# Kernel optimization log

Measured on AMD Instinct MI355X. Metric: run time of the kernel, lower is better.

The kernel has to match this reference:

```python
import jax, jax.numpy as jnp
import numpy as np

GROUPS = 4
EPS = 1e-5

def _bn(x, p, axis=1):
    # p: (4, C) rows = gamma, beta, running_mean, running_var (inference BN)
    g, b, m, v = p
    shp = [1] * x.ndim
    shp[axis] = -1
    return (x - m.reshape(shp)) * (g.reshape(shp) / jnp.sqrt(v.reshape(shp) + EPS)) + b.reshape(shp)

def _axial(x, qkv_w, bn_qkv, bn_sim, bn_out, rel, width):
    # x: (N, C, H, W). Attend along H if width=False, along W if width=True.
    if width:
        x = x.transpose(0, 2, 1, 3)   # (N, H, C, W)
    else:
        x = x.transpose(0, 3, 1, 2)   # (N, W, C, H)
    N, Wd, C, H = x.shape
    gp = C // GROUPS
    x = x.reshape(N * Wd, C, H)
    qkv = jnp.einsum('oc,bch->boh', qkv_w, x)            # 1x1 conv1d
    qkv = _bn(qkv, bn_qkv, axis=1)
    qkv = qkv.reshape(N * Wd, GROUPS, 2 * gp, H)
    q, k, v = qkv[:, :, :gp // 2], qkv[:, :, gp // 2:gp], qkv[:, :, gp:]
    i = jnp.arange(H)
    rel_idx = i[:, None] - i[None, :] + H - 1             # (H, H)
    all_emb = rel[:, rel_idx]                             # (2*gp, H, H)
    q_emb, k_emb, v_emb = all_emb[:gp // 2], all_emb[gp // 2:gp], all_emb[gp:]
    qr = jnp.einsum('bgci,cij->bgij', q, q_emb) * 0.1     # f_qr = 0.1
    kr = jnp.einsum('bgci,cij->bgij', k, k_emb).swapaxes(2, 3) * 0.1  # f_kr
    qk = jnp.einsum('bgci,bgcj->bgij', q, k)
    stacked = jnp.concatenate([qk, qr, kr], axis=1)       # (NW, 3*groups, H, H)
    stacked = _bn(stacked, bn_sim, axis=1)
    sim = stacked.reshape(N * Wd, 3, GROUPS, H, H).sum(1)
    sim = jax.nn.softmax(sim, axis=3)
    sv = jnp.einsum('bgij,bgcj->bgci', sim, v)            # f_sv = 1.0
    sve = jnp.einsum('bgij,cij->bgci', sim, v_emb) * 0.1  # f_sve = 0.1
    out = jnp.concatenate([sv, sve], axis=-1).reshape(N * Wd, 2 * C, H)
    out = _bn(out, bn_out, axis=1)
    out = out.reshape(N, Wd, C, 2, H).sum(3)              # (N, Wd, C, H)
    if width:
        return out.transpose(0, 2, 1, 3)                  # (N, C, H, W)
    return out.transpose(0, 2, 3, 1)

def _conv3x3(x, w, b):
    y = jax.lax.conv_general_dilated(x, w, (1, 1), 'SAME',
                                     dimension_numbers=('NCHW', 'OIHW', 'NCHW'))
    return y + b[None, :, None, None]

def setup_inputs() -> dict:
    key = jax.random.key(0)
    ks = jax.random.split(key, 16)
    C, KS = 256, 44
    def bn_pack(k, c):
        p = jax.random.uniform(k, (4, c), dtype=jnp.float32)
        return p.at[3].add(0.5)  # keep running_var well away from 0
    return {
        'x': jax.random.normal(ks[0], (16, C, 2 * KS, 2 * KS), jnp.float32),
        'h_qkv_w': jax.random.normal(ks[1], (2 * C, C), jnp.float32) * np.sqrt(1.0 / C),
        'h_bn_qkv': bn_pack(ks[2], 2 * C),
        'h_bn_sim': bn_pack(ks[3], 3 * GROUPS),
        'h_bn_out': bn_pack(ks[4], 2 * C),
        'h_rel': jax.random.normal(ks[5], (2 * (C // GROUPS), 2 * KS - 1), jnp.float32) * np.sqrt(GROUPS / C),
        'w_qkv_w': jax.random.normal(ks[6], (2 * C, C), jnp.float32) * np.sqrt(1.0 / C),
        'w_bn_qkv': bn_pack(ks[7], 2 * C),
        'w_bn_sim': bn_pack(ks[8], 3 * GROUPS),
        'w_bn_out': bn_pack(ks[9], 2 * C),
        'w_rel': jax.random.normal(ks[10], (2 * (C // GROUPS), 2 * KS - 1), jnp.float32) * np.sqrt(GROUPS / C),
        'conv_w': jax.random.normal(ks[11], (C, C, 3, 3), jnp.float32) * np.sqrt(1.0 / (C * 9)),
        'conv_b': jax.random.normal(ks[12], (C,), jnp.float32) * 0.01,
    }

def reference(x, h_qkv_w, h_bn_qkv, h_bn_sim, h_bn_out, h_rel,
              w_qkv_w, w_bn_qkv, w_bn_sim, w_bn_out, w_rel, conv_w, conv_b):
    B, C, H2, W2 = x.shape
    h, w = H2 // 2, W2 // 2
    # 'b c (p1 h)(p2 w) -> (b p1 p2) c h w'; same axial blocks applied to all 4 patches
    p = x.reshape(B, C, 2, h, 2, w).transpose(0, 2, 4, 1, 3, 5).reshape(B * 4, C, h, w)
    r = p
    p = _axial(p, h_qkv_w, h_bn_qkv, h_bn_sim, h_bn_out, h_rel, width=False)
    p = _axial(p, w_qkv_w, w_bn_qkv, w_bn_sim, w_bn_out, w_rel, width=True)
    p = p + r
    p = _conv3x3(p, conv_w, conv_b)
    # '(b p1 p2) c h w -> b c (p1 h)(p2 w)'
    out = p.reshape(B, 2, 2, C, h, w).transpose(0, 3, 1, 4, 2, 5).reshape(B, C, H2, W2)
    return out
```

## Files before the change

### kernel.cpp

```cpp
#include <hip/hip_runtime.h>
#include <math.h>

#define EPSV 1e-5f

typedef unsigned short u16t;
typedef unsigned int u32t;
typedef __attribute__((ext_vector_type(8))) short bf16x8;
typedef __attribute__((ext_vector_type(8))) unsigned short u16x8;
typedef __attribute__((ext_vector_type(4))) float f32x4;

#define N_P  31719424
#define N_CW 589824
#define N_QW 131072

__device__ __align__(16) u16t g_cwhi[N_CW], g_cwlo[N_CW];
__device__ __align__(16) u16t g_qwhi[2][N_QW], g_qwlo[2][N_QW];
__device__ __align__(16) u16t g_relq[2][3072];
__device__ __align__(16) u16t g_relk[2][3072];
__device__ __align__(16) u16t g_relv[2][6144];

__device__ __forceinline__ u16t f2bf_rn(float f) {
    u32t u = __float_as_uint(f);
    u32t r = u + 0x7FFFu + ((u >> 16) & 1u);
    return (u16t)(r >> 16);
}
__device__ __forceinline__ float bf2f(u16t h) {
    return __uint_as_float(((u32t)h) << 16);
}

__global__ __launch_bounds__(256)
void transpose_x(const float* __restrict__ x,
                 u16t* __restrict__ xth, u16t* __restrict__ xtl)
{
    __shared__ u16t th[64][90];
    __shared__ u16t tl[64][90];
    const int cg = blockIdx.x, yy = blockIdx.y, b = blockIdx.z;
    const int t = threadIdx.x;
    const float* src = x + ((size_t)(b * 256 + cg * 64) * 88 + yy) * 88;
    for (int e = t; e < 5632; e += 256) {
        int c = e / 88, xx = e - c * 88;
        float v = src[(size_t)c * 7744 + xx];
        u16t hi = f2bf_rn(v);
        u16t lo = f2bf_rn(v - bf2f(hi));
        th[c][xx] = hi;
        tl[c][xx] = lo;
    }
    __syncthreads();
    const int i2 = (yy >= 44);
    const int yl = yy - 44 * i2;
    for (int u = t; u < 5632; u += 256) {
        int xx = u >> 6, c = u & 63;
        int i4 = (xx >= 44);
        int xl = xx - 44 * i4;
        int n = b * 4 + i2 * 2 + i4;
        size_t idx = ((size_t)(n * 44 + yl) * 44 + xl) * 256 + cg * 64 + c;
        xth[idx] = th[c][xx];
        xtl[idx] = tl[c][xx];
    }
}

__global__ __launch_bounds__(256)
void wsplit_conv(const float* __restrict__ cw)
{
    int idx = blockIdx.x * 256 + threadIdx.x;
    if (idx >= N_CW) return;
    int tap = idx % 9;
    int rem = idx / 9;
    int ci = rem & 255, co = rem >> 8;
    float w = cw[idx];
    u16t hi = f2bf_rn(w);
    u16t lo = f2bf_rn(w - bf2f(hi));
    int cit = ci >> 5, ci5 = ci & 31, ci8 = ci5 >> 3, e = ci5 & 7;
    int didx = (((cit * 9 + tap) * 4 + ci8) * 256 + co) * 8 + e;
    g_cwhi[didx] = hi;
    g_cwlo[didx] = lo;
}

__global__ __launch_bounds__(256)
void wsplit_qkv(const float* __restrict__ wh_, const float* __restrict__ ww_)
{
    int idx = blockIdx.x * 256 + threadIdx.x;
    if (idx >= 2 * N_QW) return;
    int sel = idx >> 17;
    int id  = idx & (N_QW - 1);
    float w = (sel ? ww_ : wh_)[id];
    u16t hi = f2bf_rn(w);
    u16t lo = f2bf_rn(w - bf2f(hi));
    int o = id >> 8, c = id & 255;
    int kt = c >> 5, ci8 = (c >> 3) & 3, e = c & 7;
    int didx = ((kt * 4 + ci8) * 512 + o) * 8 + e;
    g_qwhi[sel][didx] = hi;
    g_qwlo[sel][didx] = lo;
}

__global__ __launch_bounds__(256)
void wsplit_rel(const float* __restrict__ rh, const float* __restrict__ rw)
{
    int idx = blockIdx.x * 256 + threadIdx.x;
    if (idx >= 24576) return;
    int sel = idx >= 12288;
    int id  = idx - sel * 12288;
    const float* rel = sel ? rw : rh;
    if (id < 3072) {
        int d = id >> 5, c = id & 31;
        g_relq[sel][id] = (d < 87) ? f2bf_rn(rel[c * 87 + d]) : (u16t)0;
    } else if (id < 6144) {
        int j = id - 3072;
        int d = j >> 5, c = j & 31;
        g_relk[sel][j] = (d < 87) ? f2bf_rn(rel[(32 + c) * 87 + d]) : (u16t)0;
    } else {
        int j = id - 6144;
        int c = j / 96, d = j - c * 96;
        g_relv[sel][j] = (d < 87) ? f2bf_rn(rel[(64 + c) * 87 + d]) : (u16t)0;
    }
}

#define OFF_XL 24576
#define OFF_QH 0
#define OFF_QL 3072
#define OFF_KH 6144
#define OFF_KL 9216
#define OFF_VH 12288
#define OFF_VL 20480
#define OFF_PH 28672
#define OFF_PL 34816
#define OFF_KR 28672
#define OFF_RB 40960
#define OFF_SC 50176

template<int WIDTH>
__global__ __launch_bounds__(256, 2)
void axial_kernel(const u16t* __restrict__ sh, const u16t* __restrict__ sl,
                  const u16t* __restrict__ resh, const u16t* __restrict__ resl,
                  u16t* __restrict__ outh, u16t* __restrict__ outl,
                  int sel,
                  const float* __restrict__ bnq,
                  const float* __restrict__ bns,
                  const float* __restrict__ bno)
{
    __shared__ __align__(128) char smem[62720];

    const int blk = blockIdx.x;
    const int n   = blk / 44;
    const int col = blk - n * 44;
    const int t = threadIdx.x;
    const int wv = t >> 6, lane = t & 63;
    const int l15 = lane & 15, l16 = lane >> 4;

    if (!WIDTH) {
        for (int e = t; e < 6144; e += 256) {
            int i = e >> 7, cp = e & 127;
            u32t vH = 0, vL = 0;
            if (i < 44) {
                size_t s0 = ((size_t)(n * 44 + i) * 44 + col) * 256 + cp * 2;
                vH = *(const u32t*)(sh + s0);
                vL = *(const u32t*)(sl + s0);
            }
            u32t a = ((u32t)(i * 512 + cp * 4)) ^ (((u32t)(i & 7)) << 4);
            *(u32t*)(smem + a) = vH;
            *(u32t*)(smem + OFF_XL + a) = vL;
        }
    } else {
        const u16t* ph = sh + (size_t)(n * 44 + col) * 44 * 256;
        const u16t* pl = sl + (size_t)(n * 44 + col) * 44 * 256;
        for (int e = t; e < 6144; e += 256) {
            int i = e >> 7, cp = e & 127;
            u32t vH = 0, vL = 0;
            if (i < 44) {
                vH = *(const u32t*)(ph + i * 256 + cp * 2);
                vL = *(const u32t*)(pl + i * 256 + cp * 2);
            }
            u32t a = ((u32t)(i * 512 + cp * 4)) ^ (((u32t)(i & 7)) << 4);
            *(u32t*)(smem + a) = vH;
            *(u32t*)(smem + OFF_XL + a) = vL;
        }
    }
    __syncthreads();

    f32x4 acc[8][3];
    #pragma unroll
    for (int mf = 0; mf < 8; ++mf)
        #pragma unroll
        for (int nf = 0; nf < 3; ++nf) acc[mf][nf] = (f32x4)0.f;
    {
        const u16t* WH = g_qwhi[sel];
        const u16t* WL = g_qwlo[sel];
        for (int kt = 0; kt < 8; ++kt) {
            bf16x8 bh[3], bl[3];
            #pragma unroll
            for (int nf = 0; nf < 3; ++nf) {
                int i = nf * 16 + l15;
                u32t a = ((u32t)(i * 512 + kt * 64 + l16 * 16)) ^ (((u32t)(i & 7)) << 4);
                bh[nf] = *(const bf16x8*)(smem + a);
                bl[nf] = *(const bf16x8*)(smem + OFF_XL + a);
            }
            #pragma unroll
            for (int mf = 0; mf < 8; ++mf) {
                int o = (mf * 4 + wv) * 16 + l15;
                size_t wb = ((size_t)(kt * 4 + l16) * 512 + o) * 8;
                bf16x8 ah = *(const bf16x8*)(WH + wb);
                bf16x8 al = *(const bf16x8*)(WL + wb);
                #pragma unroll
                for (int nf = 0; nf < 3; ++nf) {
                    acc[mf][nf] = __builtin_amdgcn_mfma_f32_16x16x32_bf16(ah, bh[nf], acc[mf][nf], 0, 0, 0);
                    acc[mf][nf] = __builtin_amdgcn_mfma_f32_16x16x32_bf16(al, bh[nf], acc[mf][nf], 0, 0, 0);
                    acc[mf][nf] = __builtin_amdgcn_mfma_f32_16x16x32_bf16(ah, bl[nf], acc[mf][nf], 0, 0, 0);
                }
            }
        }
    }
    __syncthreads();

    for (int e = t; e < 1280; e += 256) {
        int arr = e & 1, q = e >> 1;
        int c = q / 10, k = q - c * 10;
        u32t ad = ((u32t)(c * 128 + 88 + k * 4)) ^ (((u32t)(c & 7)) << 4);
        *(u32t*)(smem + (arr ? OFF_VL : OFF_VH) + ad) = 0;
    }

    for (int g = 0; g < 4; ++g) {
        f32x4 fq[3], fv[3];
        #pragma unroll
        for (int nf = 0; nf < 3; ++nf) { fq[nf] = acc[0][nf]; fv[nf] = acc[1][nf]; }
        #pragma unroll
        for (int m = 1; m < 4; ++m) {
            if (g == m) {
                #pragma unroll
                for (int nf = 0; nf < 3; ++nf) { fq[nf] = acc[2 * m][nf]; fv[nf] = acc[2 * m + 1][nf]; }
            }
        }

        #pragma unroll
        for (int r = 0; r < 4; ++r) {
            int ol = wv * 16 + l16 * 4 + r;
            {
                int o = g * 128 + ol;
                float s = bnq[o] * rsqrtf(bnq[1536 + o] + EPSV);
                float h = bnq[512 + o] - bnq[1024 + o] * s;
                #pragma unroll
                for (int nf = 0; nf < 3; ++nf) {
                    int i = nf * 16 + l15;
                    float val = fq[nf][r] * s + h;
                    u16t hi = f2bf_rn(val);
                    u16t lo = f2bf_rn(val - bf2f(hi));
                    if (ol < 32) {
                        u32t a = ((u32t)(i * 64 + ol * 2)) ^ (((u32t)(i & 7)) << 4);
                        *(u16t*)(smem + OFF_QH + a) = hi;
                        *(u16t*)(smem + OFF_QL + a) = lo;
                    } else {
                        int c = ol - 32;
                        u32t a = ((u32t)(i * 64 + c * 2)) ^ (((u32t)(i & 7)) << 4);
                        *(u16t*)(smem + OFF_KH + a) = hi;
                        *(u16t*)(smem + OFF_KL + a) = lo;
                    }
                }
            }
            {
                int c = ol;
                int o = g * 128 + 64 + c;
                float s = bnq[o] * rsqrtf(bnq[1536 + o] + EPSV);
                float h = bnq[512 + o] - bnq[1024 + o] * s;
                #pragma unroll
                for (int nf = 0; nf < 3; ++nf) {
                    int i = nf * 16 + l15;
                    if (i < 44) {
                        float val = fv[nf][r] * s + h;
                        u16t hi = f2bf_rn(val);
                        u16t lo = f2bf_rn(val - bf2f(hi));
                        u32t a = ((u32t)(c * 128 + i * 2)) ^ (((u32t)(c & 7)) << 4);
                        *(u16t*)(smem + OFF_VH + a) = hi;
                        *(u16t*)(smem + OFF_VL + a) = lo;
                    }
                }
            }
        }
        __syncthreads();

        for (int f = wv; f < 9; f += 4) {
            int mf = f / 3, nf = f % 3;
            int ia = mf * 16 + l15;
            u32t aq = ((u32t)(ia * 64 + l16 * 16)) ^ (((u32t)(ia & 7)) << 4);
            bf16x8 qh = *(const bf16x8*)(smem + OFF_QH + aq);
            bf16x8 ql = *(const bf16x8*)(smem + OFF_QL + aq);
            int jb = nf * 16 + l15;
            u32t ak = ((u32t)(jb * 64 + l16 * 16)) ^ (((u32t)(jb & 7)) << 4);
            bf16x8 kh = *(const bf16x8*)(smem + OFF_KH + ak);
            bf16x8 kl = *(const bf16x8*)(smem + OFF_KL + ak);
            f32x4 d = (f32x4)0.f;
            d = __builtin_amdgcn_mfma_f32_16x16x32_bf16(qh, kh, d, 0, 0, 0);
            d = __builtin_amdgcn_mfma_f32_16x16x32_bf16(ql, kh, d, 0, 0, 0);
            d = __builtin_amdgcn_mfma_f32_16x16x32_bf16(qh, kl, d, 0, 0, 0);
            #pragma unroll
            for (int r = 0; r < 4; ++r) {
                int i = mf * 16 + l16 * 4 + r;
                *(float*)(smem + OFF_SC + (i * 49 + nf * 16 + l15) * 4) = d[r];
            }
        }
        for (int f = wv; f < 18; f += 4) {
            int mf = f / 6, nf = f % 6;
            int ia = mf * 16 + l15;
            u32t aq = ((u32t)(ia * 64 + l16 * 16)) ^ (((u32t)(ia & 7)) << 4);
            bf16x8 qh = *(const bf16x8*)(smem + OFF_QH + aq);
            bf16x8 rb = *(const bf16x8*)(&g_relq[sel][(nf * 16 + l15) * 32 + l16 * 8]);
            f32x4 d = (f32x4)0.f;
            d = __builtin_amdgcn_mfma_f32_16x16x32_bf16(qh, rb, d, 0, 0, 0);
            #pragma unroll
            for (int r = 0; r < 4; ++r) {
                int i = mf * 16 + l16 * 4 + r;
                u32t a = ((u32t)(i * 192 + (nf * 16 + l15) * 2)) ^ (((u32t)(i & 7)) << 4);
                *(u16t*)(smem + OFF_RB + a) = f2bf_rn(d[r]);
            }
        }
        for (int f = wv; f < 18; f += 4) {
            int mf = f / 6, nf = f % 6;
            int ja = mf * 16 + l15;
            u32t ak = ((u32t)(ja * 64 + l16 * 16)) ^ (((u32t)(ja & 7)) << 4);
            bf16x8 kh = *(const bf16x8*)(smem + OFF_KH + ak);
            bf16x8 rb = *(const bf16x8*)(&g_relk[sel][(nf * 16 + l15) * 32 + l16 * 8]);
            f32x4 d = (f32x4)0.f;
            d = __builtin_amdgcn_mfma_f32_16x16x32_bf16(kh, rb, d, 0, 0, 0);
            #pragma unroll
            for (int r = 0; r < 4; ++r) {
                int j = mf * 16 + l16 * 4 + r;
                u32t a = ((u32t)(j * 192 + (nf * 16 + l15) * 2)) ^ (((u32t)(j & 7)) << 4);
                *(u16t*)(smem + OFF_KR + a) = f2bf_rn(d[r]);
            }
        }
        __syncthreads();

        {
            const float sqk = bns[g]     * rsqrtf(bns[36 + g] + EPSV);
            const float sqr = bns[4 + g] * rsqrtf(bns[40 + g] + EPSV);
            const float skr = bns[8 + g] * rsqrtf(bns[44 + g] + EPSV);
            for (int e = t; e < 1936; e += 256) {
                int i = e / 44, j = e - i * 44;
                int dq = i - j + 43, dk = j - i + 43;
                float scv = *(const float*)(smem + OFF_SC + (i * 49 + j) * 4);
                u16t rq = *(const u16t*)(smem + OFF_RB + (((u32t)(i * 192 + dq * 2)) ^ (((u32t)(i & 7)) << 4)));
                u16t rk = *(const u16t*)(smem + OFF_KR + (((u32t)(j * 192 + dk * 2)) ^ (((u32t)(j & 7)) << 4)));
                *(float*)(smem + OFF_SC + (i * 49 + j) * 4) =
                    sqk * scv + 0.1f * (sqr * bf2f(rq) + skr * bf2f(rk));
            }
        }
        __syncthreads();

        for (int i = wv; i < 44; i += 4) {
            float v = (lane < 44) ? *(const float*)(smem + OFF_SC + (i * 49 + lane) * 4) : -INFINITY;
            float m = v;
            #pragma unroll
            for (int off = 32; off; off >>= 1) m = fmaxf(m, __shfl_xor(m, off));
            float ex = (lane < 44) ? __expf(v - m) : 0.f;
            float ssum = ex;
            #pragma unroll
            for (int off = 32; off; off >>= 1) ssum += __shfl_xor(ssum, off);
            if (lane < 44) *(float*)(smem + OFF_SC + (i * 49 + lane) * 4) = ex / ssum;
        }
        __syncthreads();

        for (int e = t; e < 3072; e += 256) {
            int i = e >> 6, j = e & 63;
            float v = (i < 44 && j < 44) ? *(const float*)(smem + OFF_SC + (i * 49 + j) * 4) : 0.f;
            u16t hi = f2bf_rn(v);
            u16t lo = f2bf_rn(v - bf2f(hi));
            u32t a = ((u32t)(i * 128 + j * 2)) ^ (((u32t)(i & 7)) << 4);
            *(u16t*)(smem + OFF_PH + a) = hi;
            *(u16t*)(smem + OFF_PL + a) = lo;
        }
        for (int e = t; e < 4608; e += 256) {
            int i = e / 96, d = e - i * 96;
            int j = i - d + 43;
            u16t v = 0;
            if (i < 44 && j >= 0 && j < 44)
                v = f2bf_rn(*(const float*)(smem + OFF_SC + (i * 49 + j) * 4));
            u32t a = ((u32t)(i * 192 + d * 2)) ^ (((u32t)(i & 7)) << 4);
            *(u16t*)(smem + OFF_RB + a) = v;
        }
        __syncthreads();

        {
            f32x4 svf[3], svef[3];
            int fi = 0;
            for (int f = wv; f < 12; f += 4, ++fi) {
                int mf = f / 3, nf = f % 3;
                f32x4 dsv = (f32x4)0.f, dsve = (f32x4)0.f;
                #pragma unroll
                for (int kt = 0; kt < 2; ++kt) {
                    int ca = mf * 16 + l15;
                    u32t av = ((u32t)(ca * 128 + kt * 64 + l16 * 16)) ^ (((u32t)(ca & 7)) << 4);
                    bf16x8 vh = *(const bf16x8*)(smem + OFF_VH + av);
                    bf16x8 vl = *(const bf16x8*)(smem + OFF_VL + av);
                    int ib = nf * 16 + l15;
                    u32t ap = ((u32t)(ib * 128 + kt * 64 + l16 * 16)) ^ (((u32t)(ib & 7)) << 4);
                    bf16x8 ph = *(const bf16x8*)(smem + OFF_PH + ap);
                    bf16x8 pl = *(const bf16x8*)(smem + OFF_PL + ap);
                    dsv = __builtin_amdgcn_mfma_f32_16x16x32_bf16(vh, ph, dsv, 0, 0, 0);
                    dsv = __builtin_amdgcn_mfma_f32_16x16x32_bf16(vl, ph, dsv, 0, 0, 0);
                    dsv = __builtin_amdgcn_mfma_f32_16x16x32_bf16(vh, pl, dsv, 0, 0, 0);
                }
                #pragma unroll
                for (int kt = 0; kt < 3; ++kt) {
                    int ca = mf * 16 + l15;
                    bf16x8 ar = *(const bf16x8*)(&g_relv[sel][ca * 96 + kt * 32 + l16 * 8]);
                    int ib = nf * 16 + l15;
                    u32t as = ((u32t)(ib * 192 + kt * 64 + l16 * 16)) ^ (((u32t)(ib & 7)) << 4);
                    bf16x8 s2 = *(const bf16x8*)(smem + OFF_RB + as);
                    dsve = __builtin_amdgcn_mfma_f32_16x16x32_bf16(ar, s2, dsve, 0, 0, 0);
                }
                svf[fi] = dsv; svef[fi] = dsve;
            }
            __syncthreads();
            fi = 0;
            for (int f = wv; f < 12; f += 4, ++fi) {
                int mf = f / 3, nf = f % 3;
                #pragma unroll
                for (int r = 0; r < 4; ++r) {
                    int c = mf * 16 + l16 * 4 + r;
                    int o0 = g * 128 + 2 * c;
                    float s0 = bno[o0]     * rsqrtf(bno[1536 + o0] + EPSV);
                    float h0 = bno[512 + o0] - bno[1024 + o0] * s0;
                    float s1 = bno[o0 + 1] * rsqrtf(bno[1537 + o0] + EPSV);
                    float h1 = bno[513 + o0] - bno[1025 + o0] * s1;
                    int i = nf * 16 + l15;
                    float val = s0 * svf[fi][r] + h0 + s1 * (0.1f * svef[fi][r]) + h1;
                    *(float*)(smem + OFF_SC + (c * 49 + i) * 4) = val;
                }
            }
        }
        __syncthreads();

        for (int e = t; e < 2816; e += 256) {
            int c = e & 63, i = e >> 6;
            float val = *(const float*)(smem + OFF_SC + (c * 49 + i) * 4);
            int cf = g * 64 + c;
            size_t idx;
            if (!WIDTH) {
                idx = ((size_t)(n * 44 + i) * 44 + col) * 256 + cf;
            } else {
                idx = ((size_t)(n * 44 + col) * 44 + i) * 256 + cf;
                val += bf2f(resh[idx]) + bf2f(resl[idx]);
            }
            u16t hi = f2bf_rn(val);
            u16t lo = f2bf_rn(val - bf2f(hi));
            outh[idx] = hi;
            outl[idx] = lo;
        }
        __syncthreads();
    }
}

__global__ __launch_bounds__(256)
void conv_kernel(const u16t* __restrict__ phi,
                 const u16t* __restrict__ plo,
                 const float* __restrict__ cb,
                 float* __restrict__ out)
{
    __shared__ __align__(16) u16t Xs2[2][4 * 50 * 32];

    const int yb = blockIdx.x, n = blockIdx.y;
    const int y0 = yb * 2;
    const int b = n >> 2, i2 = (n >> 1) & 1, i4 = n & 1;
    const int t = threadIdx.x;
    const int wv = t >> 6, lane = t & 63;
    const int l15 = lane & 15, l16 = lane >> 4;

    f32x4 acc[4][6];
    #pragma unroll
    for (int mf = 0; mf < 4; ++mf)
        #pragma unroll
        for (int nf = 0; nf < 6; ++nf) acc[mf][nf] = (f32x4)0.f;

    char* lds = (char*)&Xs2[0][0];

    for (int cit = 0; cit < 8; ++cit) {
        const int ci0 = cit * 32;
        __syncthreads();
        for (int m = t; m < 1600; m += 256) {
            int ci8 = m & 3;
            int rem = m >> 2;
            int colm = rem % 50;
            int rr  = rem / 50;
            int arr = rr >> 2, rowidx = rr & 3;
            int gy = y0 - 1 + rowidx, gx = colm - 1;
            u16x8 v = (u16x8)0;
            if (gy >= 0 && gy < 44 && gx >= 0 && gx < 44) {
                const u16t* src = (arr ? plo : phi)
                    + (size_t)((n * 44 + gy) * 44 + gx) * 256 + ci0 + ci8 * 8;
                v = *(const u16x8*)src;
            }
            u32t addr = (u32t)((rowidx * 50 + colm) * 64 + ci8 * 16);
            addr ^= ((colm & 7) << 4);
            *(u16x8*)(lds + arr * 12800 + addr) = v;
        }
        __syncthreads();

        for (int tap = 0; tap < 9; ++tap) {
            const int dy = tap / 3, dx = tap % 3;
            const size_t wb = ((size_t)((cit * 9 + tap) * 4 + l16) * 256 + wv * 64 + l15) * 8;
            const u16x8* wh = (const u16x8*)(g_cwhi + wb);
            const u16x8* wl = (const u16x8*)(g_cwlo + wb);
            bf16x8 ah[4], al[4];
            #pragma unroll
            for (int mf = 0; mf < 4; ++mf) {
                ah[mf] = (bf16x8)wh[mf * 16];
                al[mf] = (bf16x8)wl[mf * 16];
            }
            int colr = l15 + dx;
            u32t rbase = (u32t)((dy * 50 + colr) * 64 + l16 * 16);
            rbase ^= ((colr & 7) << 4);
            const char* hb = lds + rbase;

            #pragma unroll
            for (int nf = 0; nf < 6; ++nf) {
                const int ry = nf / 3, cbk = nf % 3;
                const int off = ry * 3200 + cbk * 1024;
                bf16x8 bh = *(const bf16x8*)(hb + off);
                bf16x8 bl = *(const bf16x8*)(hb + 12800 + off);
                #pragma unroll
                for (int mf = 0; mf < 4; ++mf) {
                    acc[mf][nf] = __builtin_amdgcn_mfma_f32_16x16x32_bf16(ah[mf], bh, acc[mf][nf], 0, 0, 0);
                    acc[mf][nf] = __builtin_amdgcn_mfma_f32_16x16x32_bf16(al[mf], bh, acc[mf][nf], 0, 0, 0);
                    acc[mf][nf] = __builtin_amdgcn_mfma_f32_16x16x32_bf16(ah[mf], bl, acc[mf][nf], 0, 0, 0);
                }
            }
        }
    }

    #pragma unroll
    for (int mf = 0; mf < 4; ++mf) {
        const int cobase = wv * 64 + mf * 16 + l16 * 4;
        float bias[4];
        #pragma unroll
        for (int r = 0; r < 4; ++r) bias[r] = cb[cobase + r];
        #pragma unroll
        for (int nf = 0; nf < 6; ++nf) {
            const int ry = nf / 3, cbk = nf % 3;
            const int x = cbk * 16 + l15;
            if (x < 44) {
                const int y = y0 + ry;
                #pragma unroll
                for (int r = 0; r < 4; ++r) {
                    const int co = cobase + r;
                    out[((size_t)(b * 256 + co) * 88 + i2 * 44 + y) * 88 + i4 * 44 + x]
                        = acc[mf][nf][r] + bias[r];
                }
            }
        }
    }
}

extern "C" void kernel_launch(void* const* d_in, const int* in_sizes, int n_in,
                              void* d_out, int out_size, void* d_ws, size_t ws_size,
                              hipStream_t stream)
{
    (void)in_sizes; (void)n_in; (void)out_size; (void)ws_size;

    const float* x        = (const float*)d_in[0];
    const float* h_qkv_w  = (const float*)d_in[1];
    const float* h_bn_qkv = (const float*)d_in[2];
    const float* h_bn_sim = (const float*)d_in[3];
    const float* h_bn_out = (const float*)d_in[4];
    const float* h_rel    = (const float*)d_in[5];
    const float* w_qkv_w  = (const float*)d_in[6];
    const float* w_bn_qkv = (const float*)d_in[7];
    const float* w_bn_sim = (const float*)d_in[8];
    const float* w_bn_out = (const float*)d_in[9];
    const float* w_rel    = (const float*)d_in[10];
    const float* conv_w   = (const float*)d_in[11];
    const float* conv_b   = (const float*)d_in[12];

    u16t* xth = (u16t*)d_ws;
    u16t* xtl = xth + N_P;
    u16t* p1h = xtl + N_P;
    u16t* p1l = p1h + N_P;
    float* o  = (float*)d_out;

    transpose_x<<<dim3(4, 88, 16), 256, 0, stream>>>(x, xth, xtl);
    wsplit_conv<<<(N_CW + 255) / 256, 256, 0, stream>>>(conv_w);
    wsplit_qkv<<<(2 * N_QW + 255) / 256, 256, 0, stream>>>(h_qkv_w, w_qkv_w);
    wsplit_rel<<<96, 256, 0, stream>>>(h_rel, w_rel);

    axial_kernel<0><<<2816, 256, 0, stream>>>(xth, xtl, nullptr, nullptr, p1h, p1l,
        0, h_bn_qkv, h_bn_sim, h_bn_out);
    axial_kernel<1><<<2816, 256, 0, stream>>>(p1h, p1l, xth, xtl, p1h, p1l,
        1, w_bn_qkv, w_bn_sim, w_bn_out);
    conv_kernel<<<dim3(22, 64), 256, 0, stream>>>(p1h, p1l, conv_b, o);
}
```

Baseline: 1.780 ms.

## Restructure axial attention: precompute BN, scatter rel terms, fuse output epilogue

Folds the batch-norm scale and shift factors, including the 0.1 relative-embedding factors, into a small preprocessing kernel so the axial kernel no longer recomputes rsqrt per element. The qr/kr relative terms stay in registers and are added into the score matrix with LDS atomics, replacing the bf16 staging buffers and the separate combine pass. Softmax now writes the hi/lo probability split and the diagonal-shifted buffer directly. The output BN, residual add and stores are fused into the MFMA epilogue with vectorized writes. Less shared memory lets occupancy go from 2 to 3 blocks. The cost is LDS atomic contention and higher register pressure.

After: 2.172 ms. 1.22x slower.

```diff
diff --git a/kernel.cpp b/kernel.cpp
--- a/kernel.cpp
+++ b/kernel.cpp
@@ -7,6 +7,7 @@
 typedef unsigned int u32t;
 typedef __attribute__((ext_vector_type(8))) short bf16x8;
 typedef __attribute__((ext_vector_type(8))) unsigned short u16x8;
+typedef __attribute__((ext_vector_type(4))) unsigned short u16x4;
 typedef __attribute__((ext_vector_type(4))) float f32x4;
 
 #define N_P  31719424
@@ -18,6 +19,9 @@
 __device__ __align__(16) u16t g_relq[2][3072];
 __device__ __align__(16) u16t g_relk[2][3072];
 __device__ __align__(16) u16t g_relv[2][6144];
+__device__ __align__(16) float g_bnq_s[2][512], g_bnq_h[2][512];
+__device__ __align__(16) float g_out_s0[2][256], g_out_s1[2][256], g_out_h[2][256];
+__device__ float g_bnsf[2][12];
 
 __device__ __forceinline__ u16t f2bf_rn(float f) {
     u32t u = __float_as_uint(f);
@@ -111,7 +115,40 @@
     } else {
         int j = id - 6144;
         int c = j / 96, d = j - c * 96;
-        g_relv[sel][j] = (d < 87) ? f2bf_rn(rel[(64 + c) * 87 + d]) : (u16t)0;
+        g_relv[sel][j] = (d < 87) ? f2bf_rn(0.1f * rel[(64 + c) * 87 + d]) : (u16t)0;
+    }
+}
+
+__global__ __launch_bounds__(256)
+void wsplit_bn(const float* __restrict__ hq, const float* __restrict__ hs, const float* __restrict__ ho,
+               const float* __restrict__ wq, const float* __restrict__ ws, const float* __restrict__ wo)
+{
+    int idx = blockIdx.x * 256 + threadIdx.x;
+    if (idx >= 1560) return;
+    int sel = idx >= 780;
+    int id  = idx - sel * 780;
+    const float* bq = sel ? wq : hq;
+    const float* bs = sel ? ws : hs;
+    const float* bo = sel ? wo : ho;
+    if (id < 512) {
+        float s = bq[id] * rsqrtf(bq[1536 + id] + EPSV);
+        g_bnq_s[sel][id] = s;
+        g_bnq_h[sel][id] = bq[512 + id] - bq[1024 + id] * s;
+    } else if (id < 768) {
+        int cf = id - 512;
+        int o0 = 2 * cf, o1 = o0 + 1;
+        float s0 = bo[o0] * rsqrtf(bo[1536 + o0] + EPSV);
+        float s1 = bo[o1] * rsqrtf(bo[1536 + o1] + EPSV);
+        g_out_s0[sel][cf] = s0;
+        g_out_s1[sel][cf] = s1;
+        g_out_h[sel][cf] = (bo[512 + o0] - bo[1024 + o0] * s0)
+                         + (bo[512 + o1] - bo[1024 + o1] * s1);
+    } else {
+        int k = id - 768;
+        int gg = k & 3, which = k >> 2;
+        float s = bs[which * 4 + gg] * rsqrtf(bs[36 + which * 4 + gg] + EPSV);
+        if (which) s *= 0.1f;
+        g_bnsf[sel][which * 4 + gg] = s;
     }
 }
 
@@ -124,21 +161,17 @@
 #define OFF_VL 20480
 #define OFF_PH 28672
 #define OFF_PL 34816
-#define OFF_KR 28672
-#define OFF_RB 40960
-#define OFF_SC 50176
+#define OFF_SC 40960
+#define OFF_S2 0
 
 template<int WIDTH>
-__global__ __launch_bounds__(256, 2)
+__global__ __launch_bounds__(256, 3)
 void axial_kernel(const u16t* __restrict__ sh, const u16t* __restrict__ sl,
                   const u16t* __restrict__ resh, const u16t* __restrict__ resl,
                   u16t* __restrict__ outh, u16t* __restrict__ outl,
-                  int sel,
-                  const float* __restrict__ bnq,
-                  const float* __restrict__ bns,
-                  const float* __restrict__ bno)
-{
-    __shared__ __align__(128) char smem[62720];
+                  int sel)
+{
+    __shared__ __align__(128) char smem[50384];
 
     const int blk = blockIdx.x;
     const int n   = blk / 44;
@@ -146,6 +179,7 @@
     const int t = threadIdx.x;
     const int wv = t >> 6, lane = t & 63;
     const int l15 = lane & 15, l16 = lane >> 4;
+    float* SCf = (float*)(smem + OFF_SC);
 
     if (!WIDTH) {
         for (int e = t; e < 6144; e += 256) {
@@ -235,8 +269,7 @@
             int ol = wv * 16 + l16 * 4 + r;
             {
                 int o = g * 128 + ol;
-                float s = bnq[o] * rsqrtf(bnq[1536 + o] + EPSV);
-                float h = bnq[512 + o] - bnq[1024 + o] * s;
+                float s = g_bnq_s[sel][o], h = g_bnq_h[sel][o];
                 #pragma unroll
                 for (int nf = 0; nf < 3; ++nf) {
                     int i = nf * 16 + l15;
@@ -258,8 +291,7 @@
             {
                 int c = ol;
                 int o = g * 128 + 64 + c;
-                float s = bnq[o] * rsqrtf(bnq[1536 + o] + EPSV);
-                float h = bnq[512 + o] - bnq[1024 + o] * s;
+                float s = g_bnq_s[sel][o], h = g_bnq_h[sel][o];
                 #pragma unroll
                 for (int nf = 0; nf < 3; ++nf) {
                     int i = nf * 16 + l15;
@@ -276,76 +308,76 @@
         }
         __syncthreads();
 
-        for (int f = wv; f < 9; f += 4) {
-            int mf = f / 3, nf = f % 3;
-            int ia = mf * 16 + l15;
-            u32t aq = ((u32t)(ia * 64 + l16 * 16)) ^ (((u32t)(ia & 7)) << 4);
-            bf16x8 qh = *(const bf16x8*)(smem + OFF_QH + aq);
-            bf16x8 ql = *(const bf16x8*)(smem + OFF_QL + aq);
-            int jb = nf * 16 + l15;
-            u32t ak = ((u32t)(jb * 64 + l16 * 16)) ^ (((u32t)(jb & 7)) << 4);
-            bf16x8 kh = *(const bf16x8*)(smem + OFF_KH + ak);
-            bf16x8 kl = *(const bf16x8*)(smem + OFF_KL + ak);
-            f32x4 d = (f32x4)0.f;
-            d = __builtin_amdgcn_mfma_f32_16x16x32_bf16(qh, kh, d, 0, 0, 0);
-            d = __builtin_amdgcn_mfma_f32_16x16x32_bf16(ql, kh, d, 0, 0, 0);
-            d = __builtin_amdgcn_mfma_f32_16x16x32_bf16(qh, kl, d, 0, 0, 0);
-            #pragma unroll
-            for (int r = 0; r < 4; ++r) {
-                int i = mf * 16 + l16 * 4 + r;
-                *(float*)(smem + OFF_SC + (i * 49 + nf * 16 + l15) * 4) = d[r];
-            }
-        }
-        for (int f = wv; f < 18; f += 4) {
-            int mf = f / 6, nf = f % 6;
-            int ia = mf * 16 + l15;
-            u32t aq = ((u32t)(ia * 64 + l16 * 16)) ^ (((u32t)(ia & 7)) << 4);
-            bf16x8 qh = *(const bf16x8*)(smem + OFF_QH + aq);
-            bf16x8 rb = *(const bf16x8*)(&g_relq[sel][(nf * 16 + l15) * 32 + l16 * 8]);
-            f32x4 d = (f32x4)0.f;
-            d = __builtin_amdgcn_mfma_f32_16x16x32_bf16(qh, rb, d, 0, 0, 0);
-            #pragma unroll
-            for (int r = 0; r < 4; ++r) {
-                int i = mf * 16 + l16 * 4 + r;
-                u32t a = ((u32t)(i * 192 + (nf * 16 + l15) * 2)) ^ (((u32t)(i & 7)) << 4);
-                *(u16t*)(smem + OFF_RB + a) = f2bf_rn(d[r]);
-            }
-        }
-        for (int f = wv; f < 18; f += 4) {
-            int mf = f / 6, nf = f % 6;
-            int ja = mf * 16 + l15;
-            u32t ak = ((u32t)(ja * 64 + l16 * 16)) ^ (((u32t)(ja & 7)) << 4);
-            bf16x8 kh = *(const bf16x8*)(smem + OFF_KH + ak);
-            bf16x8 rb = *(const bf16x8*)(&g_relk[sel][(nf * 16 + l15) * 32 + l16 * 8]);
-            f32x4 d = (f32x4)0.f;
-            d = __builtin_amdgcn_mfma_f32_16x16x32_bf16(kh, rb, d, 0, 0, 0);
-            #pragma unroll
-            for (int r = 0; r < 4; ++r) {
-                int j = mf * 16 + l16 * 4 + r;
-                u32t a = ((u32t)(j * 192 + (nf * 16 + l15) * 2)) ^ (((u32t)(j & 7)) << 4);
-                *(u16t*)(smem + OFF_KR + a) = f2bf_rn(d[r]);
+        const float sqk  = g_bnsf[sel][g];
+        const float sqr1 = g_bnsf[sel][4 + g];
+        const float skr1 = g_bnsf[sel][8 + g];
+
+        #pragma unroll
+        for (int fi = 0; fi < 3; ++fi) {
+            int f = fi * 4 + wv;
+            if (f < 9) {
+                int mf = f / 3, nf = f % 3;
+                int ia = mf * 16 + l15;
+                u32t aq = ((u32t)(ia * 64 + l16 * 16)) ^ (((u32t)(ia & 7)) << 4);
+                bf16x8 qh = *(const bf16x8*)(smem + OFF_QH + aq);
+                bf16x8 ql = *(const bf16x8*)(smem + OFF_QL + aq);
+                int jb = nf * 16 + l15;
+                u32t ak = ((u32t)(jb * 64 + l16 * 16)) ^ (((u32t)(jb & 7)) << 4);
+                bf16x8 kh = *(const bf16x8*)(smem + OFF_KH + ak);
+                bf16x8 kl = *(const bf16x8*)(smem + OFF_KL + ak);
+                f32x4 d = (f32x4)0.f;
+                d = __builtin_amdgcn_mfma_f32_16x16x32_bf16(qh, kh, d, 0, 0, 0);
+                d = __builtin_amdgcn_mfma_f32_16x16x32_bf16(ql, kh, d, 0, 0, 0);
+                d = __builtin_amdgcn_mfma_f32_16x16x32_bf16(qh, kl, d, 0, 0, 0);
+                #pragma unroll
+                for (int r = 0; r < 4; ++r) {
+                    int i = mf * 16 + l16 * 4 + r;
+                    SCf[i * 49 + nf * 16 + l15] = d[r] * sqk;
+                }
+            }
+        }
+        f32x4 rfr[5], kfr[5];
+        #pragma unroll
+        for (int fi = 0; fi < 5; ++fi) {
+            int f = fi * 4 + wv;
+            if (f < 18) {
+                int mf = f / 6, nf = f % 6;
+                int ia = mf * 16 + l15;
+                u32t aq = ((u32t)(ia * 64 + l16 * 16)) ^ (((u32t)(ia & 7)) << 4);
+                bf16x8 qh = *(const bf16x8*)(smem + OFF_QH + aq);
+                bf16x8 rb = *(const bf16x8*)(&g_relq[sel][(nf * 16 + l15) * 32 + l16 * 8]);
+                f32x4 d = (f32x4)0.f;
+                rfr[fi] = __builtin_amdgcn_mfma_f32_16x16x32_bf16(qh, rb, d, 0, 0, 0);
+                u32t ak = ((u32t)(ia * 64 + l16 * 16)) ^ (((u32t)(ia & 7)) << 4);
+                bf16x8 kh = *(const bf16x8*)(smem + OFF_KH + ak);
+                bf16x8 rk = *(const bf16x8*)(&g_relk[sel][(nf * 16 + l15) * 32 + l16 * 8]);
+                f32x4 d2 = (f32x4)0.f;
+                kfr[fi] = __builtin_amdgcn_mfma_f32_16x16x32_bf16(kh, rk, d2, 0, 0, 0);
             }
         }
         __syncthreads();
 
-        {
-            const float sqk = bns[g]     * rsqrtf(bns[36 + g] + EPSV);
-            const float sqr = bns[4 + g] * rsqrtf(bns[40 + g] + EPSV);
-            const float skr = bns[8 + g] * rsqrtf(bns[44 + g] + EPSV);
-            for (int e = t; e < 1936; e += 256) {
-                int i = e / 44, j = e - i * 44;
-                int dq = i - j + 43, dk = j - i + 43;
-                float scv = *(const float*)(smem + OFF_SC + (i * 49 + j) * 4);
-                u16t rq = *(const u16t*)(smem + OFF_RB + (((u32t)(i * 192 + dq * 2)) ^ (((u32t)(i & 7)) << 4)));
-                u16t rk = *(const u16t*)(smem + OFF_KR + (((u32t)(j * 192 + dk * 2)) ^ (((u32t)(j & 7)) << 4)));
-                *(float*)(smem + OFF_SC + (i * 49 + j) * 4) =
-                    sqk * scv + 0.1f * (sqr * bf2f(rq) + skr * bf2f(rk));
+        #pragma unroll
+        for (int fi = 0; fi < 5; ++fi) {
+            int f = fi * 4 + wv;
+            if (f < 18) {
+                int mf = f / 6, nf = f % 6;
+                int dd = nf * 16 + l15;
+                #pragma unroll
+                for (int r = 0; r < 4; ++r) {
+                    int i = mf * 16 + l16 * 4 + r;
+                    int j = i - dd + 43;
+                    if (i < 44 && j >= 0 && j < 44) {
+                        atomicAdd(&SCf[i * 49 + j], rfr[fi][r] * sqr1);
+                        atomicAdd(&SCf[j * 49 + i], kfr[fi][r] * skr1);
+                    }
+                }
             }
         }
         __syncthreads();
 
         for (int i = wv; i < 44; i += 4) {
-            float v = (lane < 44) ? *(const float*)(smem + OFF_SC + (i * 49 + lane) * 4) : -INFINITY;
+            float v = (lane < 44) ? SCf[i * 49 + lane] : -INFINITY;
             float m = v;
             #pragma unroll
             for (int off = 32; off; off >>= 1) m = fmaxf(m, __shfl_xor(m, off));
@@ -353,96 +385,84 @@
             float ssum = ex;
             #pragma unroll
             for (int off = 32; off; off >>= 1) ssum += __shfl_xor(ssum, off);
-            if (lane < 44) *(float*)(smem + OFF_SC + (i * 49 + lane) * 4) = ex / ssum;
+            float p = ex / ssum;
+            u16t hi = f2bf_rn(p);
+            u16t lo = f2bf_rn(p - bf2f(hi));
+            u32t ap = ((u32t)(i * 128 + lane * 2)) ^ (((u32t)(i & 7)) << 4);
+            *(u16t*)(smem + OFF_PH + ap) = hi;
+            *(u16t*)(smem + OFF_PL + ap) = lo;
+            int j1 = i + 43 - lane;
+            float s1v = __shfl(p, j1 & 63);
+            s1v = (j1 >= 0 && j1 < 44) ? s1v : 0.f;
+            u32t a1 = ((u32t)(i * 192 + lane * 2)) ^ (((u32t)(i & 7)) << 4);
+            *(u16t*)(smem + OFF_S2 + a1) = f2bf_rn(s1v);
+            if (lane < 32) {
+                int j2 = i - 21 - lane;
+                float s2v = __shfl(p, j2 & 63);
+                s2v = (j2 >= 0) ? s2v : 0.f;
+                u32t a2 = ((u32t)(i * 192 + (lane + 64) * 2)) ^ (((u32t)(i & 7)) << 4);
+                *(u16t*)(smem + OFF_S2 + a2) = f2bf_rn(s2v);
+            }
         }
         __syncthreads();
 
-        for (int e = t; e < 3072; e += 256) {
-            int i = e >> 6, j = e & 63;
-            float v = (i < 44 && j < 44) ? *(const float*)(smem + OFF_SC + (i * 49 + j) * 4) : 0.f;
-            u16t hi = f2bf_rn(v);
-            u16t lo = f2bf_rn(v - bf2f(hi));
-            u32t a = ((u32t)(i * 128 + j * 2)) ^ (((u32t)(i & 7)) << 4);
-            *(u16t*)(smem + OFF_PH + a) = hi;
-            *(u16t*)(smem + OFF_PL + a) = lo;
-        }
-        for (int e = t; e < 4608; e += 256) {
-            int i = e / 96, d = e - i * 96;
-            int j = i - d + 43;
-            u16t v = 0;
-            if (i < 44 && j >= 0 && j < 44)
-                v = f2bf_rn(*(const float*)(smem + OFF_SC + (i * 49 + j) * 4));
-            u32t a = ((u32t)(i * 192 + d * 2)) ^ (((u32t)(i & 7)) << 4);
-            *(u16t*)(smem + OFF_RB + a) = v;
-        }
-        __syncthreads();
-
-        {
-            f32x4 svf[3], svef[3];
-            int fi = 0;
-            for (int f = wv; f < 12; f += 4, ++fi) {
-                int mf = f / 3, nf = f % 3;
-                f32x4 dsv = (f32x4)0.f, dsve = (f32x4)0.f;
-                #pragma unroll
-                for (int kt = 0; kt < 2; ++kt) {
-                    int ca = mf * 16 + l15;
-                    u32t av = ((u32t)(ca * 128 + kt * 64 + l16 * 16)) ^ (((u32t)(ca & 7)) << 4);
-                    bf16x8 vh = *(const bf16x8*)(smem + OFF_VH + av);
-                    bf16x8 vl = *(const bf16x8*)(smem + OFF_VL + av);
-                    int ib = nf * 16 + l15;
-                    u32t ap = ((u32t)(ib * 128 + kt * 64 + l16 * 16)) ^ (((u32t)(ib & 7)) << 4);
-                    bf16x8 ph = *(const bf16x8*)(smem + OFF_PH + ap);
-                    bf16x8 pl = *(const bf16x8*)(smem + OFF_PL + ap);
-                    dsv = __builtin_amdgcn_mfma_f32_16x16x32_bf16(vh, ph, dsv, 0, 0, 0);
-                    dsv = __builtin_amdgcn_mfma_f32_16x16x32_bf16(vl, ph, dsv, 0, 0, 0);
-                    dsv = __builtin_amdgcn_mfma_f32_16x16x32_bf16(vh, pl, dsv, 0, 0, 0);
-                }
-                #pragma unroll
-                for (int kt = 0; kt < 3; ++kt) {
-                    int ca = mf * 16 + l15;
-                    bf16x8 ar = *(const bf16x8*)(&g_relv[sel][ca * 96 + kt * 32 + l16 * 8]);
-                    int ib = nf * 16 + l15;
-                    u32t as = ((u32t)(ib * 192 + kt * 64 + l16 * 16)) ^ (((u32t)(ib & 7)) << 4);
-                    bf16x8 s2 = *(const bf16x8*)(smem + OFF_RB + as);
-                    dsve = __builtin_amdgcn_mfma_f32_16x16x32_bf16(ar, s2, dsve, 0, 0, 0);
-                }
-                svf[fi] = dsv; svef[fi] = dsve;
-            }
-            __syncthreads();
-            fi = 0;
-            for (int f = wv; f < 12; f += 4, ++fi) {
-                int mf = f / 3, nf = f % 3;
+        #pragma unroll
+        for (int fi = 0; fi < 3; ++fi) {
+            int f = fi * 4 + wv;
+            int mf = f / 3, nf = f % 3;
+            f32x4 dsv = (f32x4)0.f, dsve = (f32x4)0.f;
+            #pragma unroll
+            for (int kt = 0; kt < 2; ++kt) {
+                int ca = mf * 16 + l15;
+                u32t av = ((u32t)(ca * 128 + kt * 64 + l16 * 16)) ^ (((u32t)(ca & 7)) << 4);
+                bf16x8 vh = *(const bf16x8*)(smem + OFF_VH + av);
+                bf16x8 vl = *(const bf16x8*)(smem + OFF_VL + av);
+                int ib = nf * 16 + l15;
+                u32t ap = ((u32t)(ib * 128 + kt * 64 + l16 * 16)) ^ (((u32t)(ib & 7)) << 4);
+                bf16x8 ph = *(const bf16x8*)(smem + OFF_PH + ap);
+                bf16x8 pl = *(const bf16x8*)(smem + OFF_PL + ap);
+                dsv = __builtin_amdgcn_mfma_f32_16x16x32_bf16(vh, ph, dsv, 0, 0, 0);
+                dsv = __builtin_amdgcn_mfma_f32_16x16x32_bf16(vl, ph, dsv, 0, 0, 0);
+                dsv = __builtin_amdgcn_mfma_f32_16x16x32_bf16(vh, pl, dsv, 0, 0, 0);
+            }
+            #pragma unroll
+            for (int kt = 0; kt < 3; ++kt) {
+                int ca = mf * 16 + l15;
+                bf16x8 ar = *(const bf16x8*)(&g_relv[sel][ca * 96 + kt * 32 + l16 * 8]);
+                int ib = nf * 16 + l15;
+                u32t as = ((u32t)(ib * 192 + kt * 64 + l16 * 16)) ^ (((u32t)(ib & 7)) << 4);
+                bf16x8 s2 = *(const bf16x8*)(smem + OFF_S2 + as);
+                dsve = __builtin_amdgcn_mfma_f32_16x16x32_bf16(ar, s2, dsve, 0, 0, 0);
+            }
+            int i = nf * 16 + l15;
+            if (i < 44) {
+                int cf0 = g * 64 + mf * 16 + l16 * 4;
+                f32x4 s0 = *(const f32x4*)&g_out_s0[sel][cf0];
+                f32x4 s1 = *(const f32x4*)&g_out_s1[sel][cf0];
+                f32x4 hh = *(const f32x4*)&g_out_h[sel][cf0];
+                size_t idx;
+                if (!WIDTH) idx = ((size_t)(n * 44 + i) * 44 + col) * 256 + cf0;
+                else        idx = ((size_t)(n * 44 + col) * 44 + i) * 256 + cf0;
+                f32x4 val;
+                #pragma unroll
+                for (int r = 0; r < 4; ++r)
+                    val[r] = s0[r] * dsv[r] + s1[r] * dsve[r] + hh[r];
+                if (WIDTH) {
+                    u16x4 rh = *(const u16x4*)(resh + idx);
+                    u16x4 rl = *(const u16x4*)(resl + idx);
+                    #pragma unroll
+                    for (int r = 0; r < 4; ++r) val[r] += bf2f(rh[r]) + bf2f(rl[r]);
+                }
+                u16x4 oh, ol;
                 #pragma unroll
                 for (int r = 0; r < 4; ++r) {
-                    int c = mf * 16 + l16 * 4 + r;
-                    int o0 = g * 128 + 2 * c;
-                    float s0 = bno[o0]     * rsqrtf(bno[1536 + o0] + EPSV);
-                    float h0 = bno[512 + o0] - bno[1024 + o0] * s0;
-                    float s1 = bno[o0 + 1] * rsqrtf(bno[1537 + o0] + EPSV);
-                    float h1 = bno[513 + o0] - bno[1025 + o0] * s1;
-                    int i = nf * 16 + l15;
-                    float val = s0 * svf[fi][r] + h0 + s1 * (0.1f * svef[fi][r]) + h1;
-                    *(float*)(smem + OFF_SC + (c * 49 + i) * 4) = val;
-                }
-            }
-        }
-        __syncthreads();
-
-        for (int e = t; e < 2816; e += 256) {
-            int c = e & 63, i = e >> 6;
-            float val = *(const float*)(smem + OFF_SC + (c * 49 + i) * 4);
-            int cf = g * 64 + c;
-            size_t idx;
-            if (!WIDTH) {
-                idx = ((size_t)(n * 44 + i) * 44 + col) * 256 + cf;
-            } else {
-                idx = ((size_t)(n * 44 + col) * 44 + i) * 256 + cf;
-                val += bf2f(resh[idx]) + bf2f(resl[idx]);
-            }
-            u16t hi = f2bf_rn(val);
-            u16t lo = f2bf_rn(val - bf2f(hi));
-            outh[idx] = hi;
-            outl[idx] = lo;
+                    u16t hi = f2bf_rn(val[r]);
+                    oh[r] = hi;
+                    ol[r] = f2bf_rn(val[r] - bf2f(hi));
+                }
+                *(u16x4*)(outh + idx) = oh;
+                *(u16x4*)(outl + idx) = ol;
+            }
         }
         __syncthreads();
     }
@@ -578,10 +598,10 @@
     wsplit_conv<<<(N_CW + 255) / 256, 256, 0, stream>>>(conv_w);
     wsplit_qkv<<<(2 * N_QW + 255) / 256, 256, 0, stream>>>(h_qkv_w, w_qkv_w);
     wsplit_rel<<<96, 256, 0, stream>>>(h_rel, w_rel);
-
-    axial_kernel<0><<<2816, 256, 0, stream>>>(xth, xtl, nullptr, nullptr, p1h, p1l,
-        0, h_bn_qkv, h_bn_sim, h_bn_out);
-    axial_kernel<1><<<2816, 256, 0, stream>>>(p1h, p1l, xth, xtl, p1h, p1l,
-        1, w_bn_qkv, w_bn_sim, w_bn_out);
+    wsplit_bn<<<7, 256, 0, stream>>>(h_bn_qkv, h_bn_sim, h_bn_out,
+                                     w_bn_qkv, w_bn_sim, w_bn_out);
+
+    axial_kernel<0><<<2816, 256, 0, stream>>>(xth, xtl, nullptr, nullptr, p1h, p1l, 0);
+    axial_kernel<1><<<2816, 256, 0, stream>>>(p1h, p1l, xth, xtl, p1h, p1l, 1);
     conv_kernel<<<dim3(22, 64), 256, 0, stream>>>(p1h, p1l, conv_b, o);
 }
```
